# Kernel optimization log

Hardware: AMD Instinct MI355X
Metric: run time of the kernel (lower is better)

## Reference

```python
import jax, jax.numpy as jnp
import numpy as np

H, D = 16, 64  # head_num, head_dim
SCALE = 1.0 / D ** 0.5


def setup_inputs() -> dict:
    key = jax.random.key(0)
    ks = jax.random.split(key, 12)
    S, T, B, E = 2048, 2048, 2, 1024  # dec_seq, enc_seq, bs, input_dim
    return {
        "inputs": jax.random.normal(ks[0], (S, B, E), jnp.float32),
        "pos_embedding": jax.random.normal(ks[1], (T, 1, E), jnp.float32),
        "encoder_hidden_states": jax.random.normal(ks[2], (T, B, E), jnp.float32),
        "u": jax.random.normal(ks[3], (H, D), jnp.float32) * 0.02,
        "v": jax.random.normal(ks[4], (H, D), jnp.float32) * 0.02,
        "mask": jnp.zeros((S, T, 1), jnp.bool_),
        "Wkv": jax.random.normal(ks[5], (E, 2 * H * D), jnp.float32) * (E ** -0.5),
        "bkv": jnp.zeros((2 * H * D,), jnp.float32),
        "Wq": jax.random.normal(ks[6], (E, H * D), jnp.float32) * (E ** -0.5),
        "bq": jnp.zeros((H * D,), jnp.float32),
        "Wp": jax.random.normal(ks[7], (H * D, E), jnp.float32) * ((H * D) ** -0.5),
        "bp": jnp.zeros((E,), jnp.float32),
    }


def reference(inputs, pos_embedding, encoder_hidden_states, u, v, mask,
              Wkv, bkv, Wq, bq, Wp, bp):
    S, B, E = inputs.shape
    T = encoder_hidden_states.shape[0]
    # projections (fc_block == Linear)
    kv = encoder_hidden_states @ Wkv + bkv            # (T, B, 2HD)
    k, val = jnp.split(kv, 2, axis=-1)
    k = k.reshape(T, B, H, D)
    val = val.reshape(T, B, H, D)
    q = (inputs @ Wq + bq).reshape(S, B, H, D)
    q_u = q + u                                       # content bias (H, D) broadcast
    # content attention: (B, H, S, T)
    attn = jnp.einsum('sbhd,tbhd->bhst', q_u, k) * SCALE
    # mask (S, T, 1) -> (1, 1, S, T); all-False mask == original skip branch
    m = jnp.transpose(mask, (2, 0, 1))[:, None]
    attn = jnp.where(m, -jnp.inf, attn)
    attn = jax.nn.softmax(attn, axis=-1)
    # dropout is identity (eval)
    attn_vec = jnp.einsum('bhst,tbhd->sbhd', attn, val).reshape(S, B, H * D)
    return attn_vec @ Wp + bp                         # (S, B, E)
```

## Files before the change

kernel.cpp:

```cpp
#include <hip/hip_runtime.h>

#define Hh 16
#define Dd 64
#define Ss 2048
#define Tt 2048
#define Bb 2
#define Ee 1024
#define HD 1024
#define QSCALE 0.18033688011112042f

typedef __attribute__((ext_vector_type(8))) __bf16 bf16x8;
typedef __attribute__((ext_vector_type(4))) float f32x4;
typedef __attribute__((ext_vector_type(8))) unsigned short ushort8;

static __device__ __forceinline__ unsigned short f2b(float x) {
    union { float f; unsigned u; } v; v.f = x;
    unsigned r = v.u + 0x7FFFu + ((v.u >> 16) & 1u);
    return (unsigned short)(r >> 16);
}

static __device__ __forceinline__ unsigned cvtpk(float a, float b) {
    unsigned r;
    __asm__("v_cvt_pk_bf16_f32 %0, %1, %2" : "=v"(r) : "v"(a), "v"(b));
    return r;
}

static __device__ __forceinline__ void gld16(const unsigned short* g, unsigned short* l) {
    __builtin_amdgcn_global_load_lds(
        (const __attribute__((address_space(1))) unsigned int*)g,
        (__attribute__((address_space(3))) unsigned int*)l, 16, 0, 0);
}

__global__ __launch_bounds__(256) void prep(
    const float* __restrict__ enc, const float* __restrict__ inp,
    unsigned short* __restrict__ encb, unsigned short* __restrict__ inpb,
    const float* __restrict__ Wkv, const float* __restrict__ Wq, const float* __restrict__ Wp,
    unsigned short* __restrict__ Wkvt, unsigned short* __restrict__ Wqt,
    unsigned short* __restrict__ Wpt)
{
    __shared__ float tile[32][33];
    const int bx = blockIdx.x;
    const int tid = threadIdx.x;
    if (bx < 8192) {
        const int n4each = (Tt * Bb * Ee) / 4;
        int i = bx * 256 + tid;
        const float4* src; ushort4* dst; int j;
        if (i < n4each) { src = (const float4*)enc; dst = (ushort4*)encb; j = i; }
        else            { src = (const float4*)inp; dst = (ushort4*)inpb; j = i - n4each; }
        float4 v = src[j];
        ushort4 o; o.x = f2b(v.x); o.y = f2b(v.y); o.z = f2b(v.z); o.w = f2b(v.w);
        dst[j] = o;
        return;
    }
    int u = bx - 8192;
    const float* in; unsigned short* out; int C, cblk, rblk;
    if (u < 2048)      { in = Wkv; out = Wkvt; C = 2048; cblk = u & 63; rblk = u >> 6; }
    else if (u < 3072) { int v = u - 2048; in = Wq; out = Wqt; C = 1024; cblk = v & 31; rblk = v >> 5; }
    else               { int v = u - 3072; in = Wp; out = Wpt; C = 1024; cblk = v & 31; rblk = v >> 5; }
    const int R = 1024;
    int c0 = cblk * 32, r0 = rblk * 32;
    int tx = tid & 31, ty = tid >> 5;
    for (int i = ty; i < 32; i += 8)
        tile[i][tx] = in[(r0 + i) * (long)C + c0 + tx];
    __syncthreads();
    for (int i = ty; i < 32; i += 8)
        out[(c0 + i) * (long)R + r0 + tx] = f2b(tile[tx][i]);
}

__global__ __launch_bounds__(256) void transpose_v(const unsigned short* __restrict__ Vw,
                                                   unsigned short* __restrict__ Vt) {
    __shared__ unsigned short tile[64 * 65];
    int bh = blockIdx.y, t0 = blockIdx.x * 64;
    int tid = threadIdx.x;
#pragma unroll
    for (int i = 0; i < 2; i++) {
        int flat = tid + i * 256;
        int t = flat >> 3, seg = flat & 7;
        ushort8 v8 = *(const ushort8*)&Vw[(bh * 2048 + t0 + t) * 64 + seg * 8];
#pragma unroll
        for (int jj = 0; jj < 8; jj++)
            tile[(seg * 8 + jj) * 65 + t] = v8[jj];
    }
    __syncthreads();
#pragma unroll
    for (int i = 0; i < 2; i++) {
        int flat = tid + i * 256;
        int d = flat >> 3, tc = flat & 7;
        ushort8 o;
#pragma unroll
        for (int jj = 0; jj < 8; jj++)
            o[jj] = tile[d * 65 + tc * 8 + jj];
        *(ushort8*)&Vt[(bh * 64 + d) * 2048 + t0 + (tc ^ (d & 7)) * 8] = o;
    }
}

static __device__ __forceinline__ void gemm_core(
    const unsigned short* __restrict__ A, const unsigned short* __restrict__ Bt,
    int m0, int n0, unsigned short* lA, unsigned short* lB, f32x4 acc[4][4])
{
    const int tid = threadIdx.x;
    const int lane = tid & 63;
    const int wid = tid >> 6;
    const int waveM = (wid & 1) * 64, waveN = (wid >> 1) * 64;
    const int quad = lane >> 4, low = lane & 15;
#pragma unroll
    for (int i = 0; i < 4; i++)
#pragma unroll
        for (int j = 0; j < 4; j++) acc[i][j] = (f32x4)0.0f;

    for (int k0 = 0; k0 < 1024; k0 += 32) {
        __syncthreads();
        {
            int r0 = tid >> 2, s0 = tid & 3;
            int f1 = tid + 256, r1 = f1 >> 2, s1 = f1 & 3;
            gld16(&A[(m0 + r0) * 1024 + k0 + s0 * 8], &lA[tid * 8]);
            gld16(&A[(m0 + r1) * 1024 + k0 + s1 * 8], &lA[f1 * 8]);
            gld16(&Bt[(n0 + r0) * 1024 + k0 + s0 * 8], &lB[tid * 8]);
            gld16(&Bt[(n0 + r1) * 1024 + k0 + s1 * 8], &lB[f1 * 8]);
        }
        __syncthreads();
        bf16x8 af[4], bfr[4];
#pragma unroll
        for (int i = 0; i < 4; i++)
            af[i] = *(const bf16x8*)&lA[(waveM + i * 16 + low) * 32 + quad * 8];
#pragma unroll
        for (int j = 0; j < 4; j++)
            bfr[j] = *(const bf16x8*)&lB[(waveN + j * 16 + low) * 32 + quad * 8];
#pragma unroll
        for (int i = 0; i < 4; i++)
#pragma unroll
            for (int j = 0; j < 4; j++)
                acc[i][j] = __builtin_amdgcn_mfma_f32_16x16x32_bf16(af[i], bfr[j], acc[i][j], 0, 0, 0);
    }
}

__global__ __launch_bounds__(256) void gemm12(
    const unsigned short* __restrict__ encb, const unsigned short* __restrict__ Wkvt,
    const float* __restrict__ bkv,
    const unsigned short* __restrict__ inpb, const unsigned short* __restrict__ Wqt,
    const float* __restrict__ bq, const float* __restrict__ u,
    unsigned short* __restrict__ Kw, unsigned short* __restrict__ Vw,
    unsigned short* __restrict__ qw)
{
    __shared__ unsigned short lA[128 * 32];
    __shared__ unsigned short lB[128 * 32];
    const int bx = blockIdx.x;
    int z, m0, n0;
    const unsigned short *Ap, *Bp;
    if (bx < 512) { z = 0; m0 = (bx >> 4) * 128; n0 = (bx & 15) * 128; Ap = encb; Bp = Wkvt; }
    else { z = 1; int i = bx - 512; m0 = (i >> 3) * 128; n0 = (i & 7) * 128; Ap = inpb; Bp = Wqt; }
    f32x4 acc[4][4];
    gemm_core(Ap, Bp, m0, n0, lA, lB, acc);

    const int lane = threadIdx.x & 63;
    const int wid = threadIdx.x >> 6;
    const int waveM = (wid & 1) * 64, waveN = (wid >> 1) * 64;
    const int quad = lane >> 4, low = lane & 15;
#pragma unroll
    for (int i = 0; i < 4; i++) {
#pragma unroll
        for (int j = 0; j < 4; j++) {
#pragma unroll
            for (int r = 0; r < 4; r++) {
                int gm = m0 + waveM + i * 16 + quad * 4 + r;
                int gn = n0 + waveN + j * 16 + low;
                int t = gm >> 1, b = gm & 1;
                if (z == 0) {
                    float val = acc[i][j][r] + bkv[gn];
                    int c = gn;
                    if (c < HD) {
                        int h = c >> 6, d = c & 63;
                        Kw[(((b << 4) | h) * 2048 + t) * 64 + (((d >> 3) ^ (t & 7)) << 3) + (d & 7)] = f2b(val);
                    } else {
                        c -= HD;
                        int h = c >> 6, d = c & 63;
                        Vw[(((b << 4) | h) * 2048 + t) * 64 + d] = f2b(val);
                    }
                } else {
                    float val = (acc[i][j][r] + bq[gn] + u[gn]) * QSCALE;
                    int h = gn >> 6, d = gn & 63;
                    qw[(((b << 4) | h) * 2048 + t) * 64 + d] = f2b(val);
                }
            }
        }
    }
}

__global__ __launch_bounds__(256) void gemm3(
    const unsigned short* __restrict__ av, const unsigned short* __restrict__ Wpt,
    const float* __restrict__ bp, float* __restrict__ out)
{
    __shared__ unsigned short lA[128 * 32];
    __shared__ unsigned short lB[64 * 32];
    const int tid = threadIdx.x;
    const int lane = tid & 63;
    const int wid = tid >> 6;
    const int waveM = (wid & 1) * 64, waveN = (wid >> 1) * 32;
    const int m0 = blockIdx.y * 128, n0 = blockIdx.x * 64;
    const int quad = lane >> 4, low = lane & 15;

    f32x4 acc[4][2];
#pragma unroll
    for (int i = 0; i < 4; i++)
#pragma unroll
        for (int j = 0; j < 2; j++) acc[i][j] = (f32x4)0.0f;

    for (int k0 = 0; k0 < 1024; k0 += 32) {
        __syncthreads();
        {
            int r0 = tid >> 2, s0 = tid & 3;
            int f1 = tid + 256, r1 = f1 >> 2, s1 = f1 & 3;
            gld16(&av[(m0 + r0) * 1024 + k0 + s0 * 8], &lA[tid * 8]);
            gld16(&av[(m0 + r1) * 1024 + k0 + s1 * 8], &lA[f1 * 8]);
            gld16(&Wpt[(n0 + r0) * 1024 + k0 + s0 * 8], &lB[tid * 8]);
        }
        __syncthreads();
        bf16x8 af[4], bfr[2];
#pragma unroll
        for (int i = 0; i < 4; i++)
            af[i] = *(const bf16x8*)&lA[(waveM + i * 16 + low) * 32 + quad * 8];
#pragma unroll
        for (int j = 0; j < 2; j++)
            bfr[j] = *(const bf16x8*)&lB[(waveN + j * 16 + low) * 32 + quad * 8];
#pragma unroll
        for (int i = 0; i < 4; i++)
#pragma unroll
            for (int j = 0; j < 2; j++)
                acc[i][j] = __builtin_amdgcn_mfma_f32_16x16x32_bf16(af[i], bfr[j], acc[i][j], 0, 0, 0);
    }
#pragma unroll
    for (int i = 0; i < 4; i++)
#pragma unroll
        for (int j = 0; j < 2; j++)
#pragma unroll
            for (int r = 0; r < 4; r++) {
                int gm = m0 + waveM + i * 16 + quad * 4 + r;
                int gn = n0 + waveN + j * 16 + low;
                out[gm * 1024 + gn] = acc[i][j][r] + bp[gn];
            }
}

__global__ __launch_bounds__(256) void attn_kernel(
    const unsigned short* __restrict__ qw, const unsigned short* __restrict__ Kw,
    const unsigned short* __restrict__ Vt, unsigned short* __restrict__ av)
{
    __shared__ unsigned short kl[128 * 64];
    __shared__ unsigned short vt[64 * 128];
    __shared__ unsigned short pl[4][16 * 64];
    const int tid = threadIdx.x;
    const int lane = tid & 63;
    const int w = tid >> 6;
    const int quad = lane >> 4, low = lane & 15;
    const int swz = low & 7;
    const int bh = blockIdx.x & 31;
    const int s0 = (blockIdx.x >> 5) * 64;

    bf16x8 qf0, qf1;
    {
        const unsigned short* qa = &qw[(bh * 2048 + s0 + w * 16 + low) * 64];
        qf0 = *(const bf16x8*)&qa[quad * 8];
        qf1 = *(const bf16x8*)&qa[32 + quad * 8];
    }
    bf16x8 ones;
    {
        ushort8 o1;
#pragma unroll
        for (int i = 0; i < 8; i++) o1[i] = 0x3F80;
        ones = *(bf16x8*)&o1;
    }
    f32x4 o[4];
    f32x4 l_acc = (f32x4)0.0f;
#pragma unroll
    for (int j = 0; j < 4; j++) o[j] = (f32x4)0.0f;

    for (int t0 = 0; t0 < 2048; t0 += 128) {
        __syncthreads();
#pragma unroll
        for (int i = 0; i < 8; i++) {
            int fl = tid + i * 256;
            if (fl < 1024) {
                int row = fl >> 3, seg = fl & 7;
                gld16(&Kw[(bh * 2048 + t0 + row) * 64 + seg * 8], &kl[fl * 8]);
            } else {
                int c2 = fl - 1024;
                int d = c2 >> 4, seg = c2 & 15;
                gld16(&Vt[(bh * 64 + d) * 2048 + t0 + seg * 8], &vt[c2 * 8]);
            }
        }
        __syncthreads();

#pragma unroll
        for (int hf = 0; hf < 2; hf++) {
            f32x4 s[4];
#pragma unroll
            for (int jt = 0; jt < 4; jt++) {
                int r = hf * 64 + jt * 16 + low;
                bf16x8 kb0 = *(const bf16x8*)&kl[r * 64 + (quad ^ swz) * 8];
                bf16x8 kb1 = *(const bf16x8*)&kl[r * 64 + ((quad ^ 4) ^ swz) * 8];
                f32x4 a = (f32x4)0.0f;
                a = __builtin_amdgcn_mfma_f32_16x16x32_bf16(kb0, qf0, a, 0, 0, 0);
                s[jt] = __builtin_amdgcn_mfma_f32_16x16x32_bf16(kb1, qf1, a, 0, 0, 0);
            }
#pragma unroll
            for (int jt = 0; jt < 4; jt++)
#pragma unroll
                for (int r = 0; r < 4; r++)
                    s[jt][r] = __builtin_amdgcn_exp2f(s[jt][r]);

#pragma unroll
            for (int jt = 0; jt < 4; jt++) {
                int c8 = jt * 2 + (quad >> 1), half = quad & 1;
                uint2 pk;
                pk.x = cvtpk(s[jt][0], s[jt][1]);
                pk.y = cvtpk(s[jt][2], s[jt][3]);
                *(uint2*)&pl[w][low * 64 + ((c8 ^ swz) << 3) + half * 4] = pk;
            }
            __asm__ volatile("s_waitcnt lgkmcnt(0)" ::: "memory");

            bf16x8 pa0 = *(const bf16x8*)&pl[w][low * 64 + (quad ^ swz) * 8];
            bf16x8 pa1 = *(const bf16x8*)&pl[w][low * 64 + ((quad ^ 4) ^ swz) * 8];
            l_acc = __builtin_amdgcn_mfma_f32_16x16x32_bf16(pa0, ones, l_acc, 0, 0, 0);
            l_acc = __builtin_amdgcn_mfma_f32_16x16x32_bf16(pa1, ones, l_acc, 0, 0, 0);
#pragma unroll
            for (int j = 0; j < 4; j++) {
                int dr = j * 16 + low;
                bf16x8 vb0 = *(const bf16x8*)&vt[dr * 128 + hf * 64 + (quad ^ swz) * 8];
                bf16x8 vb1 = *(const bf16x8*)&vt[dr * 128 + hf * 64 + ((quad ^ 4) ^ swz) * 8];
                o[j] = __builtin_amdgcn_mfma_f32_16x16x32_bf16(pa0, vb0, o[j], 0, 0, 0);
                o[j] = __builtin_amdgcn_mfma_f32_16x16x32_bf16(pa1, vb1, o[j], 0, 0, 0);
            }
        }
    }

    int b = bh >> 4, hh = bh & 15;
#pragma unroll
    for (int j = 0; j < 4; j++) {
#pragma unroll
        for (int r = 0; r < 4; r++) {
            int sA_ = s0 + w * 16 + quad * 4 + r;
            int d = j * 16 + low;
            av[(sA_ * 2 + b) * 1024 + hh * 64 + d] = f2b(o[j][r] / l_acc[r]);
        }
    }
}

extern "C" void kernel_launch(void* const* d_in, const int* in_sizes, int n_in,
                              void* d_out, int out_size, void* d_ws, size_t ws_size,
                              hipStream_t stream)
{
    const float* inputs = (const float*)d_in[0];
    const float* enc    = (const float*)d_in[2];
    const float* u      = (const float*)d_in[3];
    const float* Wkv    = (const float*)d_in[6];
    const float* bkv    = (const float*)d_in[7];
    const float* Wq     = (const float*)d_in[8];
    const float* bq     = (const float*)d_in[9];
    const float* Wp     = (const float*)d_in[10];
    const float* bp     = (const float*)d_in[11];
    float* out = (float*)d_out;

    char* ws = (char*)d_ws;
    unsigned short* enc_b = (unsigned short*)(ws + (0ull << 20));
    unsigned short* inp_b = (unsigned short*)(ws + (8ull << 20));
    unsigned short* Wkv_t = (unsigned short*)(ws + (16ull << 20));
    unsigned short* Wq_t  = (unsigned short*)(ws + (20ull << 20));
    unsigned short* Wp_t  = (unsigned short*)(ws + (22ull << 20));
    unsigned short* Kw    = (unsigned short*)(ws + (24ull << 20));
    unsigned short* Vw    = (unsigned short*)(ws + (32ull << 20));
    unsigned short* qw    = (unsigned short*)(ws + (40ull << 20));
    unsigned short* av    = (unsigned short*)(ws + (48ull << 20));
    unsigned short* Vt    = enc_b;

    prep<<<8192 + 4096, 256, 0, stream>>>(enc, inputs, enc_b, inp_b, Wkv, Wq, Wp,
                                          Wkv_t, Wq_t, Wp_t);
    gemm12<<<768, 256, 0, stream>>>(enc_b, Wkv_t, bkv, inp_b, Wq_t, bq, u, Kw, Vw, qw);
    transpose_v<<<dim3(32, 32), 256, 0, stream>>>(Vw, Vt);
    attn_kernel<<<1024, 256, 0, stream>>>(qw, Kw, Vt, av);
    gemm3<<<dim3(16, 32), 256, 0, stream>>>(av, Wp_t, bp, out);
}
```

Baseline: 248.6 us.

## Double query rows per wave in attention and widen weight-transpose tiles

The attention kernel now gives each wave 32 query rows as two 16-row groups, so every K/V tile loaded into LDS is reused across twice as many queries. The key tile shrinks to 64 and the grid halves to 512 blocks. V fragments are loaded once per tile and shared by both groups. The weight transpose in prep uses 64x64 tiles with 16-byte vectorized stores. The trade-off is fewer blocks (possibly lower occupancy on 256 CUs), more registers per wave, and twice as many barriers per key position.

```diff
diff --git a/kernel.cpp b/kernel.cpp
--- a/kernel.cpp
+++ b/kernel.cpp
@@ -38,7 +38,7 @@
     unsigned short* __restrict__ Wkvt, unsigned short* __restrict__ Wqt,
     unsigned short* __restrict__ Wpt)
 {
-    __shared__ float tile[32][33];
+    __shared__ float tile[64][65];
     const int bx = blockIdx.x;
     const int tid = threadIdx.x;
     if (bx < 8192) {
@@ -54,17 +54,24 @@
     }
     int u = bx - 8192;
     const float* in; unsigned short* out; int C, cblk, rblk;
-    if (u < 2048)      { in = Wkv; out = Wkvt; C = 2048; cblk = u & 63; rblk = u >> 6; }
-    else if (u < 3072) { int v = u - 2048; in = Wq; out = Wqt; C = 1024; cblk = v & 31; rblk = v >> 5; }
-    else               { int v = u - 3072; in = Wp; out = Wpt; C = 1024; cblk = v & 31; rblk = v >> 5; }
+    if (u < 512)       { in = Wkv; out = Wkvt; C = 2048; cblk = u & 31; rblk = u >> 5; }
+    else if (u < 768)  { int v = u - 512; in = Wq; out = Wqt; C = 1024; cblk = v & 15; rblk = v >> 4; }
+    else               { int v = u - 768; in = Wp; out = Wpt; C = 1024; cblk = v & 15; rblk = v >> 4; }
     const int R = 1024;
-    int c0 = cblk * 32, r0 = rblk * 32;
-    int tx = tid & 31, ty = tid >> 5;
-    for (int i = ty; i < 32; i += 8)
+    int c0 = cblk * 64, r0 = rblk * 64;
+    int tx = tid & 63, ty = tid >> 6;
+    for (int i = ty; i < 64; i += 4)
         tile[i][tx] = in[(r0 + i) * (long)C + c0 + tx];
     __syncthreads();
-    for (int i = ty; i < 32; i += 8)
-        out[(c0 + i) * (long)R + r0 + tx] = f2b(tile[tx][i]);
+    int c_local = tid >> 2, g = tid & 3;
+    ushort8 o0, o1;
+#pragma unroll
+    for (int k = 0; k < 8; k++) o0[k] = f2b(tile[g * 16 + k][c_local]);
+#pragma unroll
+    for (int k = 0; k < 8; k++) o1[k] = f2b(tile[g * 16 + 8 + k][c_local]);
+    unsigned short* dst = &out[(c0 + c_local) * (long)R + r0 + g * 16];
+    *(ushort8*)dst = o0;
+    *(ushort8*)(dst + 8) = o1;
 }
 
 __global__ __launch_bounds__(256) void transpose_v(const unsigned short* __restrict__ Vw,
@@ -244,22 +251,26 @@
     const unsigned short* __restrict__ qw, const unsigned short* __restrict__ Kw,
     const unsigned short* __restrict__ Vt, unsigned short* __restrict__ av)
 {
-    __shared__ unsigned short kl[128 * 64];
-    __shared__ unsigned short vt[64 * 128];
-    __shared__ unsigned short pl[4][16 * 64];
+    __shared__ unsigned short kl[64 * 64];
+    __shared__ unsigned short vt[64 * 64];
+    __shared__ unsigned short pl[8][16 * 64];
     const int tid = threadIdx.x;
     const int lane = tid & 63;
     const int w = tid >> 6;
     const int quad = lane >> 4, low = lane & 15;
     const int swz = low & 7;
     const int bh = blockIdx.x & 31;
-    const int s0 = (blockIdx.x >> 5) * 64;
-
-    bf16x8 qf0, qf1;
+    const int s0 = (blockIdx.x >> 5) * 128;
+    const int s_wave = s0 + w * 32;
+
+    bf16x8 qA0, qA1, qB0, qB1;
     {
-        const unsigned short* qa = &qw[(bh * 2048 + s0 + w * 16 + low) * 64];
-        qf0 = *(const bf16x8*)&qa[quad * 8];
-        qf1 = *(const bf16x8*)&qa[32 + quad * 8];
+        const unsigned short* qa = &qw[(bh * 2048 + s_wave + low) * 64];
+        qA0 = *(const bf16x8*)&qa[quad * 8];
+        qA1 = *(const bf16x8*)&qa[32 + quad * 8];
+        const unsigned short* qb = qa + 16 * 64;
+        qB0 = *(const bf16x8*)&qb[quad * 8];
+        qB1 = *(const bf16x8*)&qb[32 + quad * 8];
     }
     bf16x8 ones;
     {
@@ -268,39 +279,51 @@
         for (int i = 0; i < 8; i++) o1[i] = 0x3F80;
         ones = *(bf16x8*)&o1;
     }
-    f32x4 o[4];
-    f32x4 l_acc = (f32x4)0.0f;
-#pragma unroll
-    for (int j = 0; j < 4; j++) o[j] = (f32x4)0.0f;
-
-    for (int t0 = 0; t0 < 2048; t0 += 128) {
-        __syncthreads();
-#pragma unroll
-        for (int i = 0; i < 8; i++) {
+    f32x4 oA[4], oB[4];
+    f32x4 lA_acc = (f32x4)0.0f, lB_acc = (f32x4)0.0f;
+#pragma unroll
+    for (int j = 0; j < 4; j++) { oA[j] = (f32x4)0.0f; oB[j] = (f32x4)0.0f; }
+
+    for (int t0 = 0; t0 < 2048; t0 += 64) {
+        __syncthreads();
+#pragma unroll
+        for (int i = 0; i < 2; i++) {
             int fl = tid + i * 256;
-            if (fl < 1024) {
-                int row = fl >> 3, seg = fl & 7;
-                gld16(&Kw[(bh * 2048 + t0 + row) * 64 + seg * 8], &kl[fl * 8]);
-            } else {
-                int c2 = fl - 1024;
-                int d = c2 >> 4, seg = c2 & 15;
-                gld16(&Vt[(bh * 64 + d) * 2048 + t0 + seg * 8], &vt[c2 * 8]);
-            }
-        }
-        __syncthreads();
+            int row = fl >> 3, seg = fl & 7;
+            gld16(&Kw[(bh * 2048 + t0 + row) * 64 + seg * 8], &kl[fl * 8]);
+            gld16(&Vt[(bh * 64 + row) * 2048 + t0 + seg * 8], &vt[fl * 8]);
+        }
+        __syncthreads();
+
+        f32x4 sA[4], sB[4];
+#pragma unroll
+        for (int jt = 0; jt < 4; jt++) {
+            int r = jt * 16 + low;
+            bf16x8 kb0 = *(const bf16x8*)&kl[r * 64 + (quad ^ swz) * 8];
+            bf16x8 kb1 = *(const bf16x8*)&kl[r * 64 + ((quad ^ 4) ^ swz) * 8];
+            f32x4 a = (f32x4)0.0f;
+            a = __builtin_amdgcn_mfma_f32_16x16x32_bf16(kb0, qA0, a, 0, 0, 0);
+            sA[jt] = __builtin_amdgcn_mfma_f32_16x16x32_bf16(kb1, qA1, a, 0, 0, 0);
+            f32x4 b = (f32x4)0.0f;
+            b = __builtin_amdgcn_mfma_f32_16x16x32_bf16(kb0, qB0, b, 0, 0, 0);
+            sB[jt] = __builtin_amdgcn_mfma_f32_16x16x32_bf16(kb1, qB1, b, 0, 0, 0);
+        }
+
+        bf16x8 vb0[4], vb1[4];
+#pragma unroll
+        for (int j = 0; j < 4; j++) {
+            int dr = j * 16 + low;
+            vb0[j] = *(const bf16x8*)&vt[dr * 64 + (quad ^ swz) * 8];
+            vb1[j] = *(const bf16x8*)&vt[dr * 64 + ((quad ^ 4) ^ swz) * 8];
+        }
 
 #pragma unroll
         for (int hf = 0; hf < 2; hf++) {
-            f32x4 s[4];
-#pragma unroll
-            for (int jt = 0; jt < 4; jt++) {
-                int r = hf * 64 + jt * 16 + low;
-                bf16x8 kb0 = *(const bf16x8*)&kl[r * 64 + (quad ^ swz) * 8];
-                bf16x8 kb1 = *(const bf16x8*)&kl[r * 64 + ((quad ^ 4) ^ swz) * 8];
-                f32x4 a = (f32x4)0.0f;
-                a = __builtin_amdgcn_mfma_f32_16x16x32_bf16(kb0, qf0, a, 0, 0, 0);
-                s[jt] = __builtin_amdgcn_mfma_f32_16x16x32_bf16(kb1, qf1, a, 0, 0, 0);
-            }
+            f32x4* s = hf ? sB : sA;
+            f32x4* o = hf ? oB : oA;
+            f32x4& l_acc = hf ? lB_acc : lA_acc;
+            unsigned short* plx = pl[w * 2 + hf];
+
 #pragma unroll
             for (int jt = 0; jt < 4; jt++)
 #pragma unroll
@@ -313,21 +336,18 @@
                 uint2 pk;
                 pk.x = cvtpk(s[jt][0], s[jt][1]);
                 pk.y = cvtpk(s[jt][2], s[jt][3]);
-                *(uint2*)&pl[w][low * 64 + ((c8 ^ swz) << 3) + half * 4] = pk;
+                *(uint2*)&plx[low * 64 + ((c8 ^ swz) << 3) + half * 4] = pk;
             }
             __asm__ volatile("s_waitcnt lgkmcnt(0)" ::: "memory");
 
-            bf16x8 pa0 = *(const bf16x8*)&pl[w][low * 64 + (quad ^ swz) * 8];
-            bf16x8 pa1 = *(const bf16x8*)&pl[w][low * 64 + ((quad ^ 4) ^ swz) * 8];
+            bf16x8 pa0 = *(const bf16x8*)&plx[low * 64 + (quad ^ swz) * 8];
+            bf16x8 pa1 = *(const bf16x8*)&plx[low * 64 + ((quad ^ 4) ^ swz) * 8];
             l_acc = __builtin_amdgcn_mfma_f32_16x16x32_bf16(pa0, ones, l_acc, 0, 0, 0);
             l_acc = __builtin_amdgcn_mfma_f32_16x16x32_bf16(pa1, ones, l_acc, 0, 0, 0);
 #pragma unroll
             for (int j = 0; j < 4; j++) {
-                int dr = j * 16 + low;
-                bf16x8 vb0 = *(const bf16x8*)&vt[dr * 128 + hf * 64 + (quad ^ swz) * 8];
-                bf16x8 vb1 = *(const bf16x8*)&vt[dr * 128 + hf * 64 + ((quad ^ 4) ^ swz) * 8];
-                o[j] = __builtin_amdgcn_mfma_f32_16x16x32_bf16(pa0, vb0, o[j], 0, 0, 0);
-                o[j] = __builtin_amdgcn_mfma_f32_16x16x32_bf16(pa1, vb1, o[j], 0, 0, 0);
+                o[j] = __builtin_amdgcn_mfma_f32_16x16x32_bf16(pa0, vb0[j], o[j], 0, 0, 0);
+                o[j] = __builtin_amdgcn_mfma_f32_16x16x32_bf16(pa1, vb1[j], o[j], 0, 0, 0);
             }
         }
     }
@@ -337,9 +357,10 @@
     for (int j = 0; j < 4; j++) {
 #pragma unroll
         for (int r = 0; r < 4; r++) {
-            int sA_ = s0 + w * 16 + quad * 4 + r;
+            int sA_ = s_wave + quad * 4 + r;
             int d = j * 16 + low;
-            av[(sA_ * 2 + b) * 1024 + hh * 64 + d] = f2b(o[j][r] / l_acc[r]);
+            av[(sA_ * 2 + b) * 1024 + hh * 64 + d] = f2b(oA[j][r] / lA_acc[r]);
+            av[((sA_ + 16) * 2 + b) * 1024 + hh * 64 + d] = f2b(oB[j][r] / lB_acc[r]);
         }
     }
 }
@@ -371,10 +392,10 @@
     unsigned short* av    = (unsigned short*)(ws + (48ull << 20));
     unsigned short* Vt    = enc_b;
 
-    prep<<<8192 + 4096, 256, 0, stream>>>(enc, inputs, enc_b, inp_b, Wkv, Wq, Wp,
+    prep<<<8192 + 1024, 256, 0, stream>>>(enc, inputs, enc_b, inp_b, Wkv, Wq, Wp,
                                           Wkv_t, Wq_t, Wp_t);
     gemm12<<<768, 256, 0, stream>>>(enc_b, Wkv_t, bkv, inp_b, Wq_t, bq, u, Kw, Vw, qw);
     transpose_v<<<dim3(32, 32), 256, 0, stream>>>(Vw, Vt);
-    attn_kernel<<<1024, 256, 0, stream>>>(qw, Kw, Vt, av);
+    attn_kernel<<<512, 256, 0, stream>>>(qw, Kw, Vt, av);
     gemm3<<<dim3(16, 32), 256, 0, stream>>>(av, Wp_t, bp, out);
 }
```

After: 247.3 us. No clear change (-0.5%).
